# Optimization experiments

Hardware: AMD Instinct MI355X
Metric: run time of the kernel (lower is better)

Reference implementation:

```python
import jax, jax.numpy as jnp
import numpy as np

B, L, H, E = 8, 4096, 8, 64
MODES = 64
IN_CH = H * E   # 512
OUT_CH = H * E  # 512


def setup_inputs() -> dict:
    key = jax.random.key(0)
    kq, kk, kv, kw1, kw2 = jax.random.split(key, 5)
    scale = 1.0 / (IN_CH * OUT_CH)
    return {
        "q": jax.random.normal(kq, (B, L, H, E), jnp.float32),
        "k": jax.random.normal(kk, (B, L, H, E), jnp.float32),
        "v": jax.random.normal(kv, (B, L, H, E), jnp.float32),
        "weights1": scale * jax.random.uniform(kw1, (H, E, E, MODES), jnp.float32),
        "weights2": scale * jax.random.uniform(kw2, (H, E, E, MODES), jnp.float32),
        # mode_select_method='lowest' -> lowest `modes` frequency bins, sorted
        "index_q": jnp.arange(MODES, dtype=jnp.int32),
        "index_kv": jnp.arange(MODES, dtype=jnp.int32),
    }


def reference(q, k, v, weights1, weights2, index_q, index_kv):
    # q, k: [B, L, H, E] -> [B, H, E, L]
    xq = jnp.transpose(q, (0, 2, 3, 1))
    xk = jnp.transpose(k, (0, 2, 3, 1))

    # rFFT along time, then gather the selected frequency modes
    xq_ft_ = jnp.fft.rfft(xq, axis=-1)[..., index_q]    # [B,H,E,Mq] complex64
    xk_ft_ = jnp.fft.rfft(xk, axis=-1)[..., index_kv]   # [B,H,E,Mk]

    # frequency-domain cross attention (plain complex einsum, NO conjugate)
    xqk_ft = jnp.einsum('bhex,bhey->bhxy', xq_ft_, xk_ft_)
    # 'tanh' activation applied to real and imag parts separately
    xqk_ft = jax.lax.complex(jnp.tanh(xqk_ft.real), jnp.tanh(xqk_ft.imag))

    xqkv_ft = jnp.einsum('bhxy,bhey->bhex', xqk_ft, xk_ft_)
    w = jax.lax.complex(weights1, weights2)              # [H,E,O,Mq]
    xqkvw = jnp.einsum('bhex,heox->bhox', xqkv_ft, w)    # [B,H,O,Mq]

    # scatter selected modes back into the full spectrum, then inverse rFFT
    n_freq = L // 2 + 1
    out_ft = jnp.zeros((B, H, E, n_freq), jnp.complex64).at[..., index_q].set(xqkvw)
    out = jnp.fft.irfft(out_ft / (IN_CH * OUT_CH), n=L, axis=-1)  # [B,H,E,L]
    return out
```

## Files before the change

### kernel.cpp

```cpp
#include <hip/hip_runtime.h>
#include <math.h>


#define Lt 4096
#define Ct 512
#define Mt 64

#define TWA_OFF   0u
#define TWJ_OFF   131072u
#define QFP_OFF   655360u
#define COEF_OFF  9043968u

__global__ __launch_bounds__(256) void init_tw(float* __restrict__ twa) {
  int id = blockIdx.x * 256 + threadIdx.x;
  int t = id >> 6, m = id & 63;
  int idx = (m * t) & 4095;
  float a = (float)idx * (1.0f / 2048.0f);
  float s, c;
  sincospif(a, &s, &c);
  twa[t * 128 + 2 * m]     = c;
  twa[t * 128 + 2 * m + 1] = -s;
}

__global__ __launch_bounds__(256) void init_twj(float* __restrict__ twj) {
  int id = blockIdx.x * 256 + threadIdx.x;
  int j = id >> 12, t = id & 4095;
  int m = j >> 1;
  int idx = (m * t) & 4095;
  float a = (float)idx * (1.0f / 2048.0f);
  float s, c;
  sincospif(a, &s, &c);
  twj[id] = (j & 1) ? s : c;
}

__global__ __launch_bounds__(256, 1) void dft_kernel(const float* __restrict__ q,
                                                     const float* __restrict__ k,
                                                     const float* __restrict__ twa,
                                                     float* __restrict__ qfp) {
  const int id   = blockIdx.x;
  const int b    = id & 7;
  const int src  = (id >> 3) & 1;
  const int cblk = (id >> 4) & 1;
  const int ch   = (id >> 5) & 7;
  const int mg   = (id >> 8) & 3;
  const int c    = cblk * 256 + threadIdx.x;
  const float* __restrict__ x = (src ? k : q) + (size_t)b * (Lt * Ct) + c;

  float acc[32];
#pragma unroll
  for (int j = 0; j < 32; ++j) acc[j] = 0.f;

  const int t0 = ch * 128;
  float n0 = x[(size_t)(t0)        * Ct];
  float n1 = x[(size_t)(t0 + 1024) * Ct];
  float n2 = x[(size_t)(t0 + 2048) * Ct];
  float n3 = x[(size_t)(t0 + 3072) * Ct];

  for (int t = t0; t < t0 + 128; ++t) {
    const float x0 = n0, x1 = n1, x2 = n2, x3 = n3;
    const int tn = (t + 1 < t0 + 128) ? (t + 1) : t0;
    n0 = x[(size_t)(tn)        * Ct];
    n1 = x[(size_t)(tn + 1024) * Ct];
    n2 = x[(size_t)(tn + 2048) * Ct];
    n3 = x[(size_t)(tn + 3072) * Ct];

    const float s02 = x0 + x2, s13 = x1 + x3;
    const float A0v = s02 + s13;
    const float A2v = s02 - s13;
    const float D0v = x0 - x2;
    const float D1v = x1 - x3;

    const float* __restrict__ tw = twa + t * 128 + mg * 32;
#pragma unroll
    for (int l = 0; l < 4; ++l) {
      {
        const float cc = tw[8 * l + 0], ns = tw[8 * l + 1];
        acc[8 * l + 0] = fmaf(A0v, cc, acc[8 * l + 0]);
        acc[8 * l + 1] = fmaf(A0v, ns, acc[8 * l + 1]);
      }
      {
        const float cc = tw[8 * l + 2], ns = tw[8 * l + 3];
        acc[8 * l + 2] = fmaf(D0v, cc, fmaf(D1v, ns, acc[8 * l + 2]));
        acc[8 * l + 3] = fmaf(D0v, ns, fmaf(-D1v, cc, acc[8 * l + 3]));
      }
      {
        const float cc = tw[8 * l + 4], ns = tw[8 * l + 5];
        acc[8 * l + 4] = fmaf(A2v, cc, acc[8 * l + 4]);
        acc[8 * l + 5] = fmaf(A2v, ns, acc[8 * l + 5]);
      }
      {
        const float cc = tw[8 * l + 6], ns = tw[8 * l + 7];
        acc[8 * l + 6] = fmaf(D0v, cc, fmaf(-D1v, ns, acc[8 * l + 6]));
        acc[8 * l + 7] = fmaf(D0v, ns, fmaf(D1v, cc, acc[8 * l + 7]));
      }
    }
  }

  const int chs = ch * 2 + src;
  float* __restrict__ outp = qfp + (size_t)(chs * 8 + b) * 65536 + (size_t)c * 2;
#pragma unroll
  for (int lm = 0; lm < 16; ++lm) {
    const int m = mg * 16 + lm;
    *(float2*)(outp + (size_t)m * 1024) = make_float2(acc[2 * lm], acc[2 * lm + 1]);
  }
}

__global__ __launch_bounds__(256) void attn_kernel(const float* __restrict__ qfp,
                                                   const float* __restrict__ w1,
                                                   const float* __restrict__ w2,
                                                   float* __restrict__ coefT) {
  __shared__ float QS[2][4096];
  __shared__ float KP[2][4096];

  const int bh   = blockIdx.x;
  const int b    = bh >> 3;
  const int h    = bh & 7;
  const int lane = threadIdx.x & 63;
  const int g    = threadIdx.x >> 6;

#pragma unroll 4
  for (int it = 0; it < 16; ++it) {
    const int r = g + 4 * it;
    float qre = 0.f, qim = 0.f, kre = 0.f, kim = 0.f;
#pragma unroll
    for (int ch = 0; ch < 8; ++ch) {
      const float2 vq = *(const float2*)(qfp + (size_t)((ch * 2 + 0) * 8 + b) * 65536 +
                                         (size_t)r * 1024 + (size_t)(h * 64 + lane) * 2);
      const float2 vk = *(const float2*)(qfp + (size_t)((ch * 2 + 1) * 8 + b) * 65536 +
                                         (size_t)r * 1024 + (size_t)(h * 64 + lane) * 2);
      qre += vq.x; qim += vq.y;
      kre += vk.x; kim += vk.y;
    }
    const int ad = r * 64 + (lane ^ (r & 31));
    QS[0][ad] = qre; QS[1][ad] = qim;
    KP[0][ad] = kre; KP[1][ad] = kim;
  }
  __syncthreads();

  {
    const int y = lane;
    float sr[16], si[16];
#pragma unroll
    for (int i = 0; i < 16; ++i) { sr[i] = 0.f; si[i] = 0.f; }
    for (int e = 0; e < 64; ++e) {
      const int ka = y * 64 + (e ^ (y & 31));
      const float kr = KP[0][ka], ki = KP[1][ka];
#pragma unroll
      for (int xi = 0; xi < 16; ++xi) {
        const int xx = g * 16 + xi;
        const int qa = xx * 64 + (e ^ (xx & 31));
        const float qr = QS[0][qa], qi = QS[1][qa];
        sr[xi] = fmaf(qr, kr, fmaf(-qi, ki, sr[xi]));
        si[xi] = fmaf(qr, ki, fmaf(qi, kr, si[xi]));
      }
    }
    __syncthreads();
#pragma unroll
    for (int xi = 0; xi < 16; ++xi) {
      const int xx = g * 16 + xi;
      const int ad = xx * 64 + (y ^ (xx & 31));
      QS[0][ad] = tanhf(sr[xi]);
      QS[1][ad] = tanhf(si[xi]);
    }
  }
  __syncthreads();

  {
    const int e = lane;
    float pr[16], pi[16];
#pragma unroll
    for (int i = 0; i < 16; ++i) { pr[i] = 0.f; pi[i] = 0.f; }
    for (int y = 0; y < 64; ++y) {
      const int ka = y * 64 + (e ^ (y & 31));
      const float kr = KP[0][ka], ki = KP[1][ka];
#pragma unroll
      for (int xi = 0; xi < 16; ++xi) {
        const int xx = g * 16 + xi;
        const int sa = xx * 64 + (y ^ (xx & 31));
        const float srv = QS[0][sa], siv = QS[1][sa];
        pr[xi] = fmaf(srv, kr, fmaf(-siv, ki, pr[xi]));
        pi[xi] = fmaf(srv, ki, fmaf(siv, kr, pi[xi]));
      }
    }
    __syncthreads();
#pragma unroll
    for (int xi = 0; xi < 16; ++xi) {
      const int xx = g * 16 + xi;
      const int ad = xx * 64 + (e ^ (xx & 31));
      KP[0][ad] = pr[xi];
      KP[1][ad] = pi[xi];
    }
  }
  __syncthreads();

  {
    const int xx = lane;
    float Or[16], Oi[16];
#pragma unroll
    for (int i = 0; i < 16; ++i) { Or[i] = 0.f; Oi[i] = 0.f; }
#pragma unroll 2
    for (int e = 0; e < 64; ++e) {
      const int pa = xx * 64 + (e ^ (xx & 31));
      const float ar = KP[0][pa], ai = KP[1][pa];
      const float* __restrict__ w1p = w1 + (size_t)((h * 64 + e) * 64 + g * 16) * 64 + xx;
      const float* __restrict__ w2p = w2 + (size_t)((h * 64 + e) * 64 + g * 16) * 64 + xx;
#pragma unroll
      for (int oi = 0; oi < 16; ++oi) {
        const float wr = w1p[oi * 64];
        const float wi = w2p[oi * 64];
        Or[oi] = fmaf(ar, wr, fmaf(-ai, wi, Or[oi]));
        Oi[oi] = fmaf(ar, wi, fmaf(ai, wr, Oi[oi]));
      }
    }
    const float gs = (xx == 0) ? 0x1p-30f : 0x1p-29f;
#pragma unroll
    for (int oi = 0; oi < 16; ++oi) {
      const int o = g * 16 + oi;
      coefT[(size_t)(bh * 128 + 2 * xx) * 64 + o]     =  gs * Or[oi];
      coefT[(size_t)(bh * 128 + 2 * xx + 1) * 64 + o] = -gs * Oi[oi];
    }
  }
}

__global__ __launch_bounds__(256, 1) void idft_kernel(const float* __restrict__ coefT,
                                                      const float* __restrict__ twj,
                                                      float* __restrict__ out) {
  const int bh = blockIdx.x >> 5;
  const int tc = (blockIdx.x >> 1) & 15;
  const int oh = blockIdx.x & 1;
  const int t  = tc * 256 + threadIdx.x;

  float acc[32];
#pragma unroll
  for (int i = 0; i < 32; ++i) acc[i] = 0.f;

  const float* __restrict__ crow = coefT + (size_t)bh * 8192 + oh * 32;

#pragma unroll 2
  for (int j = 0; j < 128; ++j) {
    const float twv = twj[(size_t)j * 4096 + t];
    const float* __restrict__ cj = crow + (size_t)j * 64;
#pragma unroll
    for (int qd = 0; qd < 8; ++qd) {
      const float4 c4 = *(const float4*)(cj + qd * 4);
      acc[qd * 4 + 0] = fmaf(c4.x, twv, acc[qd * 4 + 0]);
      acc[qd * 4 + 1] = fmaf(c4.y, twv, acc[qd * 4 + 1]);
      acc[qd * 4 + 2] = fmaf(c4.z, twv, acc[qd * 4 + 2]);
      acc[qd * 4 + 3] = fmaf(c4.w, twv, acc[qd * 4 + 3]);
    }
  }

  float* __restrict__ orow = out + (size_t)bh * 262144 + (size_t)(oh * 32) * 4096 + t;
#pragma unroll
  for (int ol = 0; ol < 32; ++ol) {
    orow[(size_t)ol * 4096] = acc[ol];
  }
}

extern "C" void kernel_launch(void* const* d_in, const int* in_sizes, int n_in,
                              void* d_out, int out_size, void* d_ws, size_t ws_size,
                              hipStream_t stream) {
  (void)in_sizes; (void)n_in; (void)out_size; (void)ws_size;
  const float* q  = (const float*)d_in[0];
  const float* k  = (const float*)d_in[1];
  const float* w1 = (const float*)d_in[3];
  const float* w2 = (const float*)d_in[4];
  float* ws   = (float*)d_ws;
  float* outp = (float*)d_out;

  float* twa   = ws + TWA_OFF;
  float* twj   = ws + TWJ_OFF;
  float* qfp   = ws + QFP_OFF;
  float* coefT = ws + COEF_OFF;

  init_tw<<<256, 256, 0, stream>>>(twa);
  init_twj<<<2048, 256, 0, stream>>>(twj);
  dft_kernel<<<1024, 256, 0, stream>>>(q, k, twa, qfp);
  attn_kernel<<<64, 256, 0, stream>>>(qfp, w1, w2, coefT);
  idft_kernel<<<2048, 256, 0, stream>>>(coefT, twj, outp);
}
```

Before: 365.3 us.

## Split attention kernel across query-mode quarters to raise block count

Result: faster. 332.8 us (-8.9%).

```diff
diff --git a/kernel.cpp b/kernel.cpp
--- a/kernel.cpp
+++ b/kernel.cpp
@@ -109,115 +109,124 @@
                                                    const float* __restrict__ w1,
                                                    const float* __restrict__ w2,
                                                    float* __restrict__ coefT) {
-  __shared__ float QS[2][4096];
-  __shared__ float KP[2][4096];
-
-  const int bh   = blockIdx.x;
-  const int b    = bh >> 3;
-  const int h    = bh & 7;
+  __shared__ float2 KS[4096];
+  __shared__ float2 QS[1024];
+
+  const int id = blockIdx.x;
+  const int b  = id >> 5;
+  const int h  = (id >> 2) & 7;
+  const int xq = id & 3;
+  const int bh = b * 8 + h;
+
   const int lane = threadIdx.x & 63;
   const int g    = threadIdx.x >> 6;
 
 #pragma unroll 4
   for (int it = 0; it < 16; ++it) {
-    const int r = g + 4 * it;
-    float qre = 0.f, qim = 0.f, kre = 0.f, kim = 0.f;
+    const int y = g + 4 * it;
+    float kre = 0.f, kim = 0.f;
+#pragma unroll
+    for (int ch = 0; ch < 8; ++ch) {
+      const float2 vk = *(const float2*)(qfp + (size_t)((ch * 2 + 1) * 8 + b) * 65536 +
+                                         (size_t)y * 1024 + (size_t)(h * 64 + lane) * 2);
+      kre += vk.x; kim += vk.y;
+    }
+    KS[y * 64 + (lane ^ (y & 31))] = make_float2(kre, kim);
+  }
+#pragma unroll
+  for (int it = 0; it < 4; ++it) {
+    const int xl = g + 4 * it;
+    const int m  = xq * 16 + xl;
+    float qre = 0.f, qim = 0.f;
 #pragma unroll
     for (int ch = 0; ch < 8; ++ch) {
       const float2 vq = *(const float2*)(qfp + (size_t)((ch * 2 + 0) * 8 + b) * 65536 +
-                                         (size_t)r * 1024 + (size_t)(h * 64 + lane) * 2);
-      const float2 vk = *(const float2*)(qfp + (size_t)((ch * 2 + 1) * 8 + b) * 65536 +
-                                         (size_t)r * 1024 + (size_t)(h * 64 + lane) * 2);
+                                         (size_t)m * 1024 + (size_t)(h * 64 + lane) * 2);
       qre += vq.x; qim += vq.y;
-      kre += vk.x; kim += vk.y;
-    }
-    const int ad = r * 64 + (lane ^ (r & 31));
-    QS[0][ad] = qre; QS[1][ad] = qim;
-    KP[0][ad] = kre; KP[1][ad] = kim;
+    }
+    QS[xl * 64 + (lane ^ xl)] = make_float2(qre, qim);
   }
   __syncthreads();
 
   {
     const int y = lane;
-    float sr[16], si[16];
-#pragma unroll
-    for (int i = 0; i < 16; ++i) { sr[i] = 0.f; si[i] = 0.f; }
+    float sr[4], si[4];
+#pragma unroll
+    for (int i = 0; i < 4; ++i) { sr[i] = 0.f; si[i] = 0.f; }
     for (int e = 0; e < 64; ++e) {
-      const int ka = y * 64 + (e ^ (y & 31));
-      const float kr = KP[0][ka], ki = KP[1][ka];
-#pragma unroll
-      for (int xi = 0; xi < 16; ++xi) {
-        const int xx = g * 16 + xi;
-        const int qa = xx * 64 + (e ^ (xx & 31));
-        const float qr = QS[0][qa], qi = QS[1][qa];
-        sr[xi] = fmaf(qr, kr, fmaf(-qi, ki, sr[xi]));
-        si[xi] = fmaf(qr, ki, fmaf(qi, kr, si[xi]));
+      const float2 kv = KS[y * 64 + (e ^ (y & 31))];
+#pragma unroll
+      for (int xi = 0; xi < 4; ++xi) {
+        const int xl = g * 4 + xi;
+        const float2 qv = QS[xl * 64 + (e ^ xl)];
+        sr[xi] = fmaf(qv.x, kv.x, fmaf(-qv.y, kv.y, sr[xi]));
+        si[xi] = fmaf(qv.x, kv.y, fmaf(qv.y, kv.x, si[xi]));
       }
     }
     __syncthreads();
 #pragma unroll
-    for (int xi = 0; xi < 16; ++xi) {
-      const int xx = g * 16 + xi;
-      const int ad = xx * 64 + (y ^ (xx & 31));
-      QS[0][ad] = tanhf(sr[xi]);
-      QS[1][ad] = tanhf(si[xi]);
+    for (int xi = 0; xi < 4; ++xi) {
+      const int xl = g * 4 + xi;
+      QS[xl * 64 + (y ^ xl)] = make_float2(tanhf(sr[xi]), tanhf(si[xi]));
     }
   }
   __syncthreads();
 
   {
     const int e = lane;
-    float pr[16], pi[16];
-#pragma unroll
-    for (int i = 0; i < 16; ++i) { pr[i] = 0.f; pi[i] = 0.f; }
+    float pr[4], pi[4];
+#pragma unroll
+    for (int i = 0; i < 4; ++i) { pr[i] = 0.f; pi[i] = 0.f; }
     for (int y = 0; y < 64; ++y) {
-      const int ka = y * 64 + (e ^ (y & 31));
-      const float kr = KP[0][ka], ki = KP[1][ka];
-#pragma unroll
-      for (int xi = 0; xi < 16; ++xi) {
-        const int xx = g * 16 + xi;
-        const int sa = xx * 64 + (y ^ (xx & 31));
-        const float srv = QS[0][sa], siv = QS[1][sa];
-        pr[xi] = fmaf(srv, kr, fmaf(-siv, ki, pr[xi]));
-        pi[xi] = fmaf(srv, ki, fmaf(siv, kr, pi[xi]));
+      const float2 kv = KS[y * 64 + (e ^ (y & 31))];
+#pragma unroll
+      for (int xi = 0; xi < 4; ++xi) {
+        const int xl = g * 4 + xi;
+        const float2 sv = QS[xl * 64 + (y ^ xl)];
+        pr[xi] = fmaf(sv.x, kv.x, fmaf(-sv.y, kv.y, pr[xi]));
+        pi[xi] = fmaf(sv.x, kv.y, fmaf(sv.y, kv.x, pi[xi]));
       }
     }
     __syncthreads();
 #pragma unroll
-    for (int xi = 0; xi < 16; ++xi) {
-      const int xx = g * 16 + xi;
-      const int ad = xx * 64 + (e ^ (xx & 31));
-      KP[0][ad] = pr[xi];
-      KP[1][ad] = pi[xi];
+    for (int xi = 0; xi < 4; ++xi) {
+      const int xl = g * 4 + xi;
+      KS[xl * 64 + (e ^ xl)] = make_float2(pr[xi], pi[xi]);
     }
   }
   __syncthreads();
 
   {
-    const int xx = lane;
-    float Or[16], Oi[16];
-#pragma unroll
-    for (int i = 0; i < 16; ++i) { Or[i] = 0.f; Oi[i] = 0.f; }
+    const int xs = (threadIdx.x & 3) * 4;
+    const int o  = threadIdx.x >> 2;
+    float Or[4], Oi[4];
+#pragma unroll
+    for (int i = 0; i < 4; ++i) { Or[i] = 0.f; Oi[i] = 0.f; }
+
+    const float* __restrict__ w1p = w1 + ((size_t)(h * 64) * 64 + o) * 64 + xq * 16 + xs;
+    const float* __restrict__ w2p = w2 + ((size_t)(h * 64) * 64 + o) * 64 + xq * 16 + xs;
+
 #pragma unroll 2
     for (int e = 0; e < 64; ++e) {
-      const int pa = xx * 64 + (e ^ (xx & 31));
-      const float ar = KP[0][pa], ai = KP[1][pa];
-      const float* __restrict__ w1p = w1 + (size_t)((h * 64 + e) * 64 + g * 16) * 64 + xx;
-      const float* __restrict__ w2p = w2 + (size_t)((h * 64 + e) * 64 + g * 16) * 64 + xx;
-#pragma unroll
-      for (int oi = 0; oi < 16; ++oi) {
-        const float wr = w1p[oi * 64];
-        const float wi = w2p[oi * 64];
-        Or[oi] = fmaf(ar, wr, fmaf(-ai, wi, Or[oi]));
-        Oi[oi] = fmaf(ar, wi, fmaf(ai, wr, Oi[oi]));
-      }
-    }
-    const float gs = (xx == 0) ? 0x1p-30f : 0x1p-29f;
-#pragma unroll
-    for (int oi = 0; oi < 16; ++oi) {
-      const int o = g * 16 + oi;
-      coefT[(size_t)(bh * 128 + 2 * xx) * 64 + o]     =  gs * Or[oi];
-      coefT[(size_t)(bh * 128 + 2 * xx + 1) * 64 + o] = -gs * Oi[oi];
+      const float4 a1 = *(const float4*)(w1p + (size_t)e * 4096);
+      const float4 a2 = *(const float4*)(w2p + (size_t)e * 4096);
+      const float wr[4] = {a1.x, a1.y, a1.z, a1.w};
+      const float wi[4] = {a2.x, a2.y, a2.z, a2.w};
+#pragma unroll
+      for (int j = 0; j < 4; ++j) {
+        const int xl = xs + j;
+        const float2 pv = KS[xl * 64 + (e ^ xl)];
+        Or[j] = fmaf(pv.x, wr[j], fmaf(-pv.y, wi[j], Or[j]));
+        Oi[j] = fmaf(pv.x, wi[j], fmaf(pv.y, wr[j], Oi[j]));
+      }
+    }
+
+#pragma unroll
+    for (int j = 0; j < 4; ++j) {
+      const int xg = xq * 16 + xs + j;
+      const float gs = (xg == 0) ? 0x1p-30f : 0x1p-29f;
+      coefT[(size_t)(bh * 128 + 2 * xg) * 64 + o]     =  gs * Or[j];
+      coefT[(size_t)(bh * 128 + 2 * xg + 1) * 64 + o] = -gs * Oi[j];
     }
   }
 }
@@ -276,6 +285,6 @@
   init_tw<<<256, 256, 0, stream>>>(twa);
   init_twj<<<2048, 256, 0, stream>>>(twj);
   dft_kernel<<<1024, 256, 0, stream>>>(q, k, twa, qfp);
-  attn_kernel<<<64, 256, 0, stream>>>(qfp, w1, w2, coefT);
+  attn_kernel<<<256, 256, 0, stream>>>(qfp, w1, w2, coefT);
   idft_kernel<<<2048, 256, 0, stream>>>(coefT, twj, outp);
 }
```
